# Performance work log

Hardware: AMD Instinct MI355X
Metric: run time of the kernel (lower is better)

## Reference

```python
import jax, jax.numpy as jnp
import numpy as np

KDIM = 8192
EPS = 1e-8  # F.cosine_similarity default eps


def _encoder(x, W1, b1, W2, b2, W3, b3):
    # x: [..., KDIM] -> [..., 128]; Linear(KDIM,512)->ReLU->Linear(512,256)->ReLU->Linear(256,128)
    h = jax.nn.relu(x @ W1 + b1)
    h = jax.nn.relu(h @ W2 + b2)
    return h @ W3 + b3


def setup_inputs() -> dict:
    key = jax.random.key(0)
    ks = jax.random.split(key, 16)

    def lin(k, fan_in, fan_out):
        bound = 1.0 / np.sqrt(fan_in)
        kw, kb = jax.random.split(k)
        W = jax.random.uniform(kw, (fan_in, fan_out), jnp.float32, -bound, bound)
        b = jax.random.uniform(kb, (fan_out,), jnp.float32, -bound, bound)
        return W, b

    W1, b1 = lin(ks[0], KDIM, 512)
    W2, b2 = lin(ks[1], 512, 256)
    W3, b3 = lin(ks[2], 256, 128)
    Wi1, bi1 = lin(ks[3], 128 + 6, 64)
    Wi2, bi2 = lin(ks[4], 64, 32)
    Wi3, bi3 = lin(ks[5], 32, 1)

    return {
        "new_knowledge": jax.random.normal(ks[6], (KDIM,), jnp.float32),
        "existing_knowledge": jax.random.normal(ks[7], (10, KDIM), jnp.float32),
        "math_metrics": jax.random.uniform(ks[8], (6,), jnp.float32),
        "W1": W1, "b1": b1, "W2": W2, "b2": b2, "W3": W3, "b3": b3,
        "Wi1": Wi1, "bi1": bi1, "Wi2": Wi2, "bi2": bi2, "Wi3": Wi3, "bi3": bi3,
    }


def reference(new_knowledge, existing_knowledge, math_metrics,
              W1, b1, W2, b2, W3, b3, Wi1, bi1, Wi2, bi2, Wi3, bi3):
    # Encode new knowledge: [128]
    new_enc = _encoder(new_knowledge, W1, b1, W2, b2, W3, b3)
    # Batched encode of the (up to 10) existing knowledge vectors: [10, 128]
    ex_enc = _encoder(existing_knowledge, W1, b1, W2, b2, W3, b3)

    # Per-item geometric distance (L2 norm of difference)
    diff = new_enc[None, :] - ex_enc                     # [10, 128]
    geo_dist = jnp.sqrt(jnp.sum(diff * diff, axis=-1))   # [10]

    # Per-item cosine similarity with torch eps clamping
    new_n = jnp.maximum(jnp.linalg.norm(new_enc), EPS)
    ex_n = jnp.maximum(jnp.linalg.norm(ex_enc, axis=-1), EPS)  # [10]
    cos = (ex_enc @ new_enc) / (new_n * ex_n)            # [10]

    avg_consistency = jnp.mean(geo_dist - cos)

    # Mathematical-constraint integrator MLP on [128 + 6]
    combined = jnp.concatenate([new_enc, math_metrics])  # [134]
    h = jax.nn.relu(combined @ Wi1 + bi1)
    h = jax.nn.relu(h @ Wi2 + bi2)
    quality = h @ Wi3 + bi3                              # [1]

    integration_loss = jnp.exp(-quality)                 # [1]
    total = jnp.squeeze(avg_consistency + integration_loss)
    return total
```

## Files before the change

### kernel.cpp

```cpp
#include <hip/hip_runtime.h>
#include <math.h>

#define EPS 1e-8f

__device__ __forceinline__ float wredsum(float v) {
#pragma unroll
  for (int o = 32; o > 0; o >>= 1) v += __shfl_down(v, o, 64);
  return v;
}

__global__ __launch_bounds__(256) void k_l1(const float* __restrict__ xn,
                                            const float* __restrict__ xe,
                                            const float* __restrict__ W1,
                                            float* __restrict__ p1,
                                            int* __restrict__ bars) {
  if (blockIdx.x == 0 && blockIdx.y == 0 && threadIdx.x == 0) bars[0] = 0;
  __shared__ float red[11 * 16 * 65];
  const int cg  = threadIdx.x & 15;
  const int ks  = threadIdx.x >> 4;
  const int col = blockIdx.x * 64 + cg * 4;
  const int k0  = blockIdx.y * 256 + ks * 16;

  float4 acc[11];
#pragma unroll
  for (int r = 0; r < 11; ++r) acc[r] = make_float4(0.f, 0.f, 0.f, 0.f);

#pragma unroll 8
  for (int i = 0; i < 16; ++i) {
    const int k = k0 + i;
    const float4 w = *(const float4*)&W1[(size_t)k * 512 + col];
    float xv = xn[k];
    acc[0].x = fmaf(xv, w.x, acc[0].x); acc[0].y = fmaf(xv, w.y, acc[0].y);
    acc[0].z = fmaf(xv, w.z, acc[0].z); acc[0].w = fmaf(xv, w.w, acc[0].w);
#pragma unroll
    for (int r = 0; r < 10; ++r) {
      const float xr = xe[r * 8192 + k];
      acc[r + 1].x = fmaf(xr, w.x, acc[r + 1].x);
      acc[r + 1].y = fmaf(xr, w.y, acc[r + 1].y);
      acc[r + 1].z = fmaf(xr, w.z, acc[r + 1].z);
      acc[r + 1].w = fmaf(xr, w.w, acc[r + 1].w);
    }
  }

#pragma unroll
  for (int r = 0; r < 11; ++r) {
    const int base = (r * 16 + ks) * 65 + cg * 4;
    red[base]     = acc[r].x; red[base + 1] = acc[r].y;
    red[base + 2] = acc[r].z; red[base + 3] = acc[r].w;
  }
  __syncthreads();
  if (threadIdx.x < 176) {
    const int r = threadIdx.x >> 4;
    const int c = threadIdx.x & 15;
    float4 s = make_float4(0.f, 0.f, 0.f, 0.f);
#pragma unroll
    for (int k = 0; k < 16; ++k) {
      const int b = (r * 16 + k) * 65 + c * 4;
      s.x += red[b]; s.y += red[b + 1]; s.z += red[b + 2]; s.w += red[b + 3];
    }
    *(float4*)&p1[((size_t)blockIdx.y * 11 + r) * 512 + blockIdx.x * 64 + c * 4] = s;
  }
}

__global__ __launch_bounds__(1024) void k_tail(
    const float* __restrict__ p1, const float* __restrict__ b1,
    const float* __restrict__ W2, const float* __restrict__ b2,
    const float* __restrict__ W3, const float* __restrict__ b3,
    const float* __restrict__ mm,
    const float* __restrict__ Wi1, const float* __restrict__ bi1,
    const float* __restrict__ Wi2, const float* __restrict__ bi2,
    const float* __restrict__ Wi3, const float* __restrict__ bi3,
    float* __restrict__ p2, int* __restrict__ bars, float* __restrict__ out) {
  __shared__ float h1sl[11 * 64];
  __shared__ float red[11264];
  __shared__ float h2s[11 * 256];
  __shared__ __align__(16) float wi1s[134 * 64];
  __shared__ float encs[1408];
  __shared__ float comb[134];
  __shared__ float h1b[64];
  __shared__ int won;
  const int t = threadIdx.x;
  const int j = blockIdx.x;

  if (t < 704) {
    const int r = t >> 6, kk = t & 63;
    const int col = j * 64 + kk;
    float s = b1[col];
#pragma unroll
    for (int ch = 0; ch < 32; ++ch) s += p1[(size_t)ch * 5632 + r * 512 + col];
    h1sl[r * 64 + kk] = fmaxf(s, 0.f);
  }
  __syncthreads();

  {
    const int col = t & 255, g = t >> 8;
    float acc[11];
#pragma unroll
    for (int r = 0; r < 11; ++r) acc[r] = 0.f;
#pragma unroll
    for (int kk = 0; kk < 16; ++kk) {
      const int kl = g * 16 + kk;
      const float w = W2[(size_t)(j * 64 + kl) * 256 + col];
#pragma unroll
      for (int r = 0; r < 11; ++r) acc[r] = fmaf(h1sl[r * 64 + kl], w, acc[r]);
    }
#pragma unroll
    for (int r = 0; r < 11; ++r) red[(g * 11 + r) * 256 + col] = acc[r];
  }
  __syncthreads();
  for (int o = t; o < 2816; o += 1024) {
    const int col = o & 255, r = o >> 8;
    p2[j * 2816 + o] = red[r * 256 + col] + red[(11 + r) * 256 + col] +
                       red[(22 + r) * 256 + col] + red[(33 + r) * 256 + col];
  }

  __syncthreads();
  if (t == 0) {
    __threadfence();
    const int old = __hip_atomic_fetch_add(bars, 1, __ATOMIC_ACQ_REL,
                                           __HIP_MEMORY_SCOPE_AGENT);
    won = (old == 7);
    if (won) __threadfence();
  }
  __syncthreads();
  if (!won) return;

  for (int i = t; i < 2144; i += 1024)
    *(float4*)&wi1s[i * 4] = *(const float4*)&Wi1[(size_t)i * 4];
  for (int o = t; o < 2816; o += 1024) {
    float s = b2[o & 255];
#pragma unroll
    for (int jj = 0; jj < 8; ++jj) s += p2[jj * 2816 + o];
    h2s[o] = fmaxf(s, 0.f);
  }
  __syncthreads();

  {
    const int c = t & 127, g = t >> 7;
    float acc[11];
#pragma unroll
    for (int r = 0; r < 11; ++r) acc[r] = 0.f;
#pragma unroll
    for (int kk = 0; kk < 32; ++kk) {
      const int k = g * 32 + kk;
      const float w = W3[(size_t)k * 128 + c];
#pragma unroll
      for (int r = 0; r < 11; ++r) acc[r] = fmaf(h2s[r * 256 + k], w, acc[r]);
    }
#pragma unroll
    for (int r = 0; r < 11; ++r) red[(g * 11 + r) * 128 + c] = acc[r];
  }
  __syncthreads();
  for (int o = t; o < 1408; o += 1024) {
    const int c = o & 127, r = o >> 7;
    float s = b3[c];
#pragma unroll
    for (int g = 0; g < 8; ++g) s += red[(g * 11 + r) * 128 + c];
    encs[o] = s;
  }
  __syncthreads();

  float consist = 0.f;
  float n0 = 0.f, n1 = 0.f;
  if (t < 64) {
    n0 = encs[t]; n1 = encs[64 + t];
    comb[t] = n0; comb[64 + t] = n1;
    if (t < 6) comb[128 + t] = mm[t];
  }
  __syncthreads();
  if (t < 64) {
    const float nn = wredsum(n0 * n0 + n1 * n1);
#pragma unroll
    for (int r = 1; r <= 10; ++r) {
      const float e0 = encs[r * 128 + t];
      const float e1 = encs[r * 128 + 64 + t];
      const float d0 = e0 - n0, d1 = e1 - n1;
      const float g  = wredsum(d0 * d0 + d1 * d1);
      const float q  = wredsum(e0 * e0 + e1 * e1);
      const float dd = wredsum(e0 * n0 + e1 * n1);
      if (t == 0) {
        const float geo = sqrtf(g);
        const float den = fmaxf(sqrtf(nn), EPS) * fmaxf(sqrtf(q), EPS);
        consist += geo - dd / den;
      }
    }
  } else if (t < 128) {
    const int tt = t - 64;
    float h = bi1[tt];
#pragma unroll 4
    for (int k = 0; k < 134; ++k) h = fmaf(comb[k], wi1s[k * 64 + tt], h);
    h1b[tt] = fmaxf(h, 0.f);
  }
  __syncthreads();
  if (t < 64) {
    float part = 0.f;
    if (t < 32) {
      float h2 = bi2[t];
#pragma unroll 8
      for (int k = 0; k < 64; ++k) h2 = fmaf(h1b[k], Wi2[k * 32 + t], h2);
      part = fmaxf(h2, 0.f) * Wi3[t];
    }
    const float qual = wredsum(part);
    if (t == 0) out[0] = consist * 0.1f + expf(-(qual + bi3[0]));
  }
}

extern "C" void kernel_launch(void* const* d_in, const int* in_sizes, int n_in,
                              void* d_out, int out_size, void* d_ws, size_t ws_size,
                              hipStream_t stream) {
  (void)in_sizes; (void)n_in; (void)out_size; (void)ws_size;
  const float* xn  = (const float*)d_in[0];
  const float* xe  = (const float*)d_in[1];
  const float* mm  = (const float*)d_in[2];
  const float* W1  = (const float*)d_in[3];
  const float* b1  = (const float*)d_in[4];
  const float* W2  = (const float*)d_in[5];
  const float* b2  = (const float*)d_in[6];
  const float* W3  = (const float*)d_in[7];
  const float* b3  = (const float*)d_in[8];
  const float* Wi1 = (const float*)d_in[9];
  const float* bi1 = (const float*)d_in[10];
  const float* Wi2 = (const float*)d_in[11];
  const float* bi2 = (const float*)d_in[12];
  const float* Wi3 = (const float*)d_in[13];
  const float* bi3 = (const float*)d_in[14];
  float* out = (float*)d_out;

  char* ws = (char*)d_ws;
  float* p1   = (float*)(ws);
  float* p2   = (float*)(ws + 720896);
  int*   bars = (int*)  (ws + 811008);

  hipLaunchKernelGGL(k_l1,   dim3(8, 32), dim3(256),  0, stream, xn, xe, W1, p1, bars);
  hipLaunchKernelGGL(k_tail, dim3(8),     dim3(1024), 0, stream,
                     p1, b1, W2, b2, W3, b3, mm,
                     Wi1, bi1, Wi2, bi2, Wi3, bi3, p2, bars, out);
}
```

Baseline: 120.5 us.

## Retile layer-1 GEMV: more blocks, preload W1 rows, vectorized x loads

```diff
diff --git a/kernel.cpp b/kernel.cpp
--- a/kernel.cpp
+++ b/kernel.cpp
@@ -9,56 +9,62 @@
   return v;
 }
 
-__global__ __launch_bounds__(256) void k_l1(const float* __restrict__ xn,
-                                            const float* __restrict__ xe,
-                                            const float* __restrict__ W1,
-                                            float* __restrict__ p1,
-                                            int* __restrict__ bars) {
+__device__ __forceinline__ void fma8(const float4* w, const float4 a,
+                                     const float4 b, float4& c) {
+  const float xs[8] = {a.x, a.y, a.z, a.w, b.x, b.y, b.z, b.w};
+#pragma unroll
+  for (int i = 0; i < 8; ++i) {
+    c.x = fmaf(xs[i], w[i].x, c.x);
+    c.y = fmaf(xs[i], w[i].y, c.y);
+    c.z = fmaf(xs[i], w[i].z, c.z);
+    c.w = fmaf(xs[i], w[i].w, c.w);
+  }
+}
+
+__global__ __launch_bounds__(256, 2) void k_l1(const float* __restrict__ xn,
+                                               const float* __restrict__ xe,
+                                               const float* __restrict__ W1,
+                                               float* __restrict__ p1,
+                                               int* __restrict__ bars) {
   if (blockIdx.x == 0 && blockIdx.y == 0 && threadIdx.x == 0) bars[0] = 0;
-  __shared__ float red[11 * 16 * 65];
-  const int cg  = threadIdx.x & 15;
-  const int ks  = threadIdx.x >> 4;
-  const int col = blockIdx.x * 64 + cg * 4;
-  const int k0  = blockIdx.y * 256 + ks * 16;
+  __shared__ float red[11 * 32 * 36];
+  const int cg  = threadIdx.x & 7;
+  const int ks  = threadIdx.x >> 3;
+  const int col = blockIdx.x * 32 + cg * 4;
+  const int k0  = blockIdx.y * 256 + ks * 8;
+
+  float4 w[8];
+#pragma unroll
+  for (int i = 0; i < 8; ++i)
+    w[i] = *(const float4*)&W1[(size_t)(k0 + i) * 512 + col];
 
   float4 acc[11];
 #pragma unroll
   for (int r = 0; r < 11; ++r) acc[r] = make_float4(0.f, 0.f, 0.f, 0.f);
 
-#pragma unroll 8
-  for (int i = 0; i < 16; ++i) {
-    const int k = k0 + i;
-    const float4 w = *(const float4*)&W1[(size_t)k * 512 + col];
-    float xv = xn[k];
-    acc[0].x = fmaf(xv, w.x, acc[0].x); acc[0].y = fmaf(xv, w.y, acc[0].y);
-    acc[0].z = fmaf(xv, w.z, acc[0].z); acc[0].w = fmaf(xv, w.w, acc[0].w);
-#pragma unroll
-    for (int r = 0; r < 10; ++r) {
-      const float xr = xe[r * 8192 + k];
-      acc[r + 1].x = fmaf(xr, w.x, acc[r + 1].x);
-      acc[r + 1].y = fmaf(xr, w.y, acc[r + 1].y);
-      acc[r + 1].z = fmaf(xr, w.z, acc[r + 1].z);
-      acc[r + 1].w = fmaf(xr, w.w, acc[r + 1].w);
-    }
-  }
-
-#pragma unroll
-  for (int r = 0; r < 11; ++r) {
-    const int base = (r * 16 + ks) * 65 + cg * 4;
-    red[base]     = acc[r].x; red[base + 1] = acc[r].y;
-    red[base + 2] = acc[r].z; red[base + 3] = acc[r].w;
-  }
-  __syncthreads();
-  if (threadIdx.x < 176) {
-    const int r = threadIdx.x >> 4;
-    const int c = threadIdx.x & 15;
-    float4 s = make_float4(0.f, 0.f, 0.f, 0.f);
-#pragma unroll
-    for (int k = 0; k < 16; ++k) {
-      const int b = (r * 16 + k) * 65 + c * 4;
-      s.x += red[b]; s.y += red[b + 1]; s.z += red[b + 2]; s.w += red[b + 3];
-    }
-    *(float4*)&p1[((size_t)blockIdx.y * 11 + r) * 512 + blockIdx.x * 64 + c * 4] = s;
+  {
+    const float4 a = *(const float4*)&xn[k0];
+    const float4 b = *(const float4*)&xn[k0 + 4];
+    fma8(w, a, b, acc[0]);
+  }
+#pragma unroll
+  for (int r = 0; r < 10; ++r) {
+    const float4 a = *(const float4*)&xe[r * 8192 + k0];
+    const float4 b = *(const float4*)&xe[r * 8192 + k0 + 4];
+    fma8(w, a, b, acc[r + 1]);
+  }
+
+#pragma unroll
+  for (int r = 0; r < 11; ++r)
+    *(float4*)&red[(r * 32 + ks) * 36 + cg * 4] = acc[r];
+  __syncthreads();
+
+  for (int o = threadIdx.x; o < 352; o += 256) {
+    const int r = o >> 5, c = o & 31;
+    float s = 0.f;
+#pragma unroll
+    for (int k = 0; k < 32; ++k) s += red[(r * 32 + k) * 36 + c];
+    p1[((size_t)blockIdx.y * 11 + r) * 512 + blockIdx.x * 32 + c] = s;
   }
 }
 
@@ -231,8 +237,8 @@
   float* p2   = (float*)(ws + 720896);
   int*   bars = (int*)  (ws + 811008);
 
-  hipLaunchKernelGGL(k_l1,   dim3(8, 32), dim3(256),  0, stream, xn, xe, W1, p1, bars);
-  hipLaunchKernelGGL(k_tail, dim3(8),     dim3(1024), 0, stream,
+  hipLaunchKernelGGL(k_l1,   dim3(16, 32), dim3(256),  0, stream, xn, xe, W1, p1, bars);
+  hipLaunchKernelGGL(k_tail, dim3(8),      dim3(1024), 0, stream,
                      p1, b1, W2, b2, W3, b3, mm,
                      Wi1, bi1, Wi2, bi2, Wi3, bi3, p2, bars, out);
 }
```

Measured after the change: 114.8 us. -4.7%, faster.
